# Kernel optimization log

Hardware: AMD Instinct MI355X
Metric: run time of the kernel (lower is better)

Reference implementation:

```python
import jax, jax.numpy as jnp
import numpy as np

B, S, D = 4, 2048, 1024


def setup_inputs() -> dict:
    key = jax.random.key(0)
    k1, k2 = jax.random.split(key)
    x = jax.random.normal(k1, (B, S, D), dtype=jnp.float32)
    W_qkv = jax.random.normal(k2, (D, 3 * D), dtype=jnp.float32) * 0.02
    # causal mask: 1 where attendable, 0 where masked (broadcast over batch)
    attention_mask = jnp.tril(jnp.ones((S, S), dtype=jnp.int32))[None, :, :]
    return {"input": x, "W_qkv": W_qkv, "attention_mask": attention_mask}


def reference(input, W_qkv, attention_mask):
    # fused QKV projection (nn.Linear, bias=False)
    qkv = jnp.einsum('bsd,de->bse', input, W_qkv)  # [B, S, 3D]
    q, k, v = jnp.split(qkv, 3, axis=-1)           # each [B, S, D]
    scale = 1.0 / jnp.sqrt(jnp.asarray(D, dtype=input.dtype))
    scores = jnp.einsum('bqd,bkd->bqk', q, k) * scale  # [B, S, S]
    neg_inf = jnp.finfo(scores.dtype).min
    scores = jnp.where(attention_mask == 0, neg_inf, scores)
    attn = jax.nn.softmax(scores, axis=-1)
    # dropout prob = 0.0 -> identity
    out = jnp.einsum('bqk,bkd->bqd', attn, v)      # [B, S, D]
    return out
```

## Files before the change

kernel.cpp:

```cpp
#include <hip/hip_runtime.h>
#include <hip/hip_bf16.h>


typedef __attribute__((ext_vector_type(8))) short short8;
typedef __attribute__((ext_vector_type(4))) short s16x4;
typedef __attribute__((ext_vector_type(4))) float f32x4;

__device__ __forceinline__ short f2bf(float f) {
  __hip_bfloat16 h = __float2bfloat16(f);
  return *reinterpret_cast<short*>(&h);
}

__device__ __forceinline__ void gll16(const void* g, void* l) {
  __builtin_amdgcn_global_load_lds((const __attribute__((address_space(1))) void*)g,
                                   (__attribute__((address_space(3))) void*)l,
                                   16, 0, 0);
}

__device__ __forceinline__ void gemm_core(const short* __restrict__ A,
                                          const short* __restrict__ Bt,
                                          int lda, int ldb,
                                          int row0, int col0, int kIters,
                                          f32x4 acc[4][4],
                                          short* lA, short* lB) {
  const int tid  = threadIdx.x;
  const int wave = tid >> 6;
  const int lane = tid & 63;
  const int quad = lane >> 4;
  const int l16  = lane & 15;

  const f32x4 zero = {0.f, 0.f, 0.f, 0.f};
#pragma unroll
  for (int i = 0; i < 4; ++i)
#pragma unroll
    for (int j = 0; j < 4; ++j) acc[i][j] = zero;

  const int srow = tid >> 3;
  const int gcol = ((tid & 7) ^ (srow & 7)) * 8;
  const short* A1 = A + (size_t)(row0 + srow) * lda + gcol;
  const short* A2 = A + (size_t)(row0 + srow + 32) * lda + gcol;
  const short* A3 = A + (size_t)(row0 + srow + 64) * lda + gcol;
  const short* A4 = A + (size_t)(row0 + srow + 96) * lda + gcol;
  const short* B1 = Bt + (size_t)(col0 + srow) * ldb + gcol;
  const short* B2 = Bt + (size_t)(col0 + srow + 32) * ldb + gcol;
  const short* B3 = Bt + (size_t)(col0 + srow + 64) * ldb + gcol;
  const short* B4 = Bt + (size_t)(col0 + srow + 96) * ldb + gcol;

  short* lA1 = lA + wave * 512;
  short* lA2 = lA + 2048 + wave * 512;
  short* lA3 = lA + 4096 + wave * 512;
  short* lA4 = lA + 6144 + wave * 512;
  short* lB1 = lB + wave * 512;
  short* lB2 = lB + 2048 + wave * 512;
  short* lB3 = lB + 4096 + wave * 512;
  short* lB4 = lB + 6144 + wave * 512;

  const int rswz  = l16 & 7;
  const int slot0 = (quad ^ rswz) * 8;
  const int slot1 = ((4 + quad) ^ rswz) * 8;
  const short* aRow = lA + ((wave >> 1) * 64 + l16) * 64;
  const short* bRow = lB + ((wave & 1) * 64 + l16) * 64;

  for (int it = 0; it < kIters; ++it) {
    const int k0 = it * 64;
    gll16(A1 + k0, lA1);
    gll16(A2 + k0, lA2);
    gll16(A3 + k0, lA3);
    gll16(A4 + k0, lA4);
    gll16(B1 + k0, lB1);
    gll16(B2 + k0, lB2);
    gll16(B3 + k0, lB3);
    gll16(B4 + k0, lB4);
    __syncthreads();

#pragma unroll
    for (int s = 0; s < 2; ++s) {
      const int so = s ? slot1 : slot0;
      short8 af[4], bfr[4];
#pragma unroll
      for (int i = 0; i < 4; ++i) af[i] = *(const short8*)(aRow + i * 1024 + so);
#pragma unroll
      for (int j = 0; j < 4; ++j) bfr[j] = *(const short8*)(bRow + j * 1024 + so);
#pragma unroll
      for (int i = 0; i < 4; ++i)
#pragma unroll
        for (int j = 0; j < 4; ++j)
          acc[i][j] = __builtin_amdgcn_mfma_f32_16x16x32_bf16(af[i], bfr[j], acc[i][j], 0, 0, 0);
    }
    __syncthreads();
  }
}

#define EPILOGUE_VARS                         \
  const int lane = threadIdx.x & 63;          \
  const int wave = threadIdx.x >> 6;          \
  const int quad = lane >> 4;                 \
  const int l16  = lane & 15;                 \
  const int rb   = (wave >> 1) * 64;          \
  const int cb   = (wave & 1) * 64;

__global__ __launch_bounds__(256) void setup_kernel(const float* __restrict__ X,
                                                    const float* __restrict__ W,
                                                    short* __restrict__ Xb,
                                                    short* __restrict__ Wt,
                                                    float* __restrict__ rs) {
  const int bid = blockIdx.x;
  if (bid < 8192) {
    const int i = (bid * 256 + threadIdx.x) * 4;
    const f32x4 v = *(const f32x4*)(X + i);
    s16x4 o;
    o.x = f2bf(v.x); o.y = f2bf(v.y); o.z = f2bf(v.z); o.w = f2bf(v.w);
    *(s16x4*)(Xb + i) = o;
  } else if (bid < 11264) {
    __shared__ float tile[32][33];
    const int r  = bid - 8192;
    const int ni = r % 96;
    const int ki = r / 96;
    const int tx = threadIdx.x & 31;
    const int ty = threadIdx.x >> 5;
#pragma unroll
    for (int rr = 0; rr < 4; ++rr)
      tile[ty + rr * 8][tx] = W[(size_t)(ki * 32 + ty + rr * 8) * 3072 + ni * 32 + tx];
    __syncthreads();
#pragma unroll
    for (int rr = 0; rr < 4; ++rr)
      Wt[(size_t)(ni * 32 + ty + rr * 8) * 1024 + ki * 32 + tx] = f2bf(tile[tx][ty + rr * 8]);
  } else {
    const int i = (bid - 11264) * 1024 + threadIdx.x * 4;
    const f32x4 zero = {0.f, 0.f, 0.f, 0.f};
    *(f32x4*)(rs + i) = zero;
  }
}

__global__ __launch_bounds__(256) void qkv_gemm_kernel(const short* __restrict__ Xb,
                                                       const short* __restrict__ Wt,
                                                       short* __restrict__ Q,
                                                       short* __restrict__ K,
                                                       short* __restrict__ Vt) {
  __shared__ short lA[8192], lB[8192];
  const int br = blockIdx.x / 24;
  const int bc = blockIdx.x % 24;
  f32x4 acc[4][4];
  gemm_core(Xb, Wt, 1024, 1024, br * 128, bc * 128, 16, acc, lA, lB);

  EPILOGUE_VARS
  const int rbase = br * 128 + rb;
  const int cbase = bc * 128 + cb;
  if (bc < 16) {
#pragma unroll
    for (int i = 0; i < 4; ++i)
#pragma unroll
      for (int j = 0; j < 4; ++j) {
        const int col = cbase + j * 16 + l16;
        short* dst = (col < 1024) ? Q : K;
        const int n = col & 1023;
#pragma unroll
        for (int r = 0; r < 4; ++r) {
          const int row = rbase + i * 16 + quad * 4 + r;
          dst[(size_t)row * 1024 + n] = f2bf(acc[i][j][r]);
        }
      }
  } else {
    const int b  = rbase >> 11;
    const int s0 = rbase & 2047;
    short* VtB = Vt + (size_t)b * 1024 * 2048;
#pragma unroll
    for (int i = 0; i < 4; ++i) {
      const int sb = s0 + i * 16 + quad * 4;
#pragma unroll
      for (int j = 0; j < 4; ++j) {
        const int d = cbase - 2048 + j * 16 + l16;
        s16x4 pk;
        pk.x = f2bf(acc[i][j][0]);
        pk.y = f2bf(acc[i][j][1]);
        pk.z = f2bf(acc[i][j][2]);
        pk.w = f2bf(acc[i][j][3]);
        *(s16x4*)(VtB + (size_t)d * 2048 + sb) = pk;
      }
    }
  }
}

__global__ __launch_bounds__(256) void qk_kernel(const short* __restrict__ Q,
                                                 const short* __restrict__ K,
                                                 short* __restrict__ E,
                                                 float* __restrict__ rs) {
  __shared__ short lA[8192], lB[8192];
  const int b  = blockIdx.x / 136;
  const int tt = blockIdx.x % 136;
  int qi = 0;
  while ((qi + 1) * (qi + 2) / 2 <= tt) qi++;
  const int ki = tt - qi * (qi + 1) / 2;

  f32x4 acc[4][4];
  const short* Qb = Q + (size_t)b * 2048 * 1024;
  const short* Kb = K + (size_t)b * 2048 * 1024;
  gemm_core(Qb, Kb, 1024, 1024, qi * 128, ki * 128, 16, acc, lA, lB);

  EPILOGUE_VARS
  short* Eb  = E + (size_t)b * 2048 * 2048;
  float* rsb = rs + b * 2048;
  const int rbase = qi * 128 + rb;
  const int cbase = ki * 128 + cb;
  const bool diag = (qi == ki);
#pragma unroll
  for (int i = 0; i < 4; ++i)
#pragma unroll
    for (int r = 0; r < 4; ++r) {
      const int row = rbase + i * 16 + quad * 4 + r;
      float partial = 0.f;
#pragma unroll
      for (int j = 0; j < 4; ++j) {
        const int col = cbase + j * 16 + l16;
        float e = __expf(acc[i][j][r] * 0.03125f);
        if (diag && col > row) e = 0.f;
        partial += e;
        Eb[(size_t)row * 2048 + col] = f2bf(e);
      }
      partial += __shfl_xor(partial, 1);
      partial += __shfl_xor(partial, 2);
      partial += __shfl_xor(partial, 4);
      partial += __shfl_xor(partial, 8);
      if (l16 == 0) atomicAdd(rsb + row, partial);
    }
}

__global__ __launch_bounds__(256) void pv_gemm_kernel(const short* __restrict__ E,
                                                      const short* __restrict__ Vt,
                                                      const float* __restrict__ rs,
                                                      float* __restrict__ out) {
  const int b  = blockIdx.x >> 7;
  const int r  = blockIdx.x & 127;
  const int qi = 15 - (r >> 3);
  const int dj = r & 7;

  __shared__ short lA[8192], lB[8192];
  f32x4 acc[4][4];
  const short* Eb  = E + (size_t)b * 2048 * 2048;
  const short* Vtb = Vt + (size_t)b * 1024 * 2048;
  gemm_core(Eb, Vtb, 2048, 2048, qi * 128, dj * 128, (qi + 1) * 2, acc, lA, lB);

  EPILOGUE_VARS
  float* ob = out + (size_t)b * 2048 * 1024;
  const float* rsb = rs + b * 2048;
  const int rbase = qi * 128 + rb;
  const int cbase = dj * 128 + cb;
#pragma unroll
  for (int i = 0; i < 4; ++i)
#pragma unroll
    for (int r2 = 0; r2 < 4; ++r2) {
      const int row = rbase + i * 16 + quad * 4 + r2;
      const float inv = 1.f / rsb[row];
#pragma unroll
      for (int j = 0; j < 4; ++j) {
        const int col = cbase + j * 16 + l16;
        ob[(size_t)row * 1024 + col] = acc[i][j][r2] * inv;
      }
    }
}

extern "C" void kernel_launch(void* const* d_in, const int* in_sizes, int n_in,
                              void* d_out, int out_size, void* d_ws, size_t ws_size,
                              hipStream_t stream) {
  const float* X = (const float*)d_in[0];
  const float* W = (const float*)d_in[1];
  float* out = (float*)d_out;
  char* w = (char*)d_ws;

  short* Xb = (short*)(w + 0);
  short* Wt = (short*)(w + 16777216);
  short* E  = (short*)(w + 0);
  float* rs = (float*)(w + 50331648);
  short* Q  = (short*)(w + 67108864);
  short* K  = (short*)(w + 83886080);
  short* Vt = (short*)(w + 100663296);

  hipLaunchKernelGGL(setup_kernel,    dim3(11272), dim3(256), 0, stream, X, W, Xb, Wt, rs);
  hipLaunchKernelGGL(qkv_gemm_kernel, dim3(1536),  dim3(256), 0, stream, Xb, Wt, Q, K, Vt);
  hipLaunchKernelGGL(qk_kernel,       dim3(544),   dim3(256), 0, stream, Q, K, E, rs);
  hipLaunchKernelGGL(pv_gemm_kernel,  dim3(512),   dim3(256), 0, stream, E, Vt, rs, out);
}
```

Measured before the change: 255.4 us.

## Fuse QK and PV kernels with per-row-block counters for cross-stage overlap

Merges the score/exp kernel and the PV GEMM into a single launch. The first 544 blocks compute QK tiles in descending query-block order and bump a per-(batch, query-block) counter with release semantics. The remaining blocks spin on that counter before running the PV GEMM for that row block. This removes a kernel boundary and lets PV work for the long rows start while QK for short rows is still running, at the cost of spin-waiting blocks that occupy CUs and rely on scheduling order to avoid deadlock. It also changes block ordering and interleaves batches.

Measured after the change: 407.7 us. +59.6%, slower.

```diff
diff --git a/kernel.cpp b/kernel.cpp
--- a/kernel.cpp
+++ b/kernel.cpp
@@ -103,7 +103,8 @@
                                                     const float* __restrict__ W,
                                                     short* __restrict__ Xb,
                                                     short* __restrict__ Wt,
-                                                    float* __restrict__ rs) {
+                                                    float* __restrict__ rs,
+                                                    int* __restrict__ cnt) {
   const int bid = blockIdx.x;
   if (bid < 8192) {
     const int i = (bid * 256 + threadIdx.x) * 4;
@@ -125,10 +126,12 @@
 #pragma unroll
     for (int rr = 0; rr < 4; ++rr)
       Wt[(size_t)(ni * 32 + ty + rr * 8) * 1024 + ki * 32 + tx] = f2bf(tile[tx][ty + rr * 8]);
-  } else {
+  } else if (bid < 11272) {
     const int i = (bid - 11264) * 1024 + threadIdx.x * 4;
     const f32x4 zero = {0.f, 0.f, 0.f, 0.f};
     *(f32x4*)(rs + i) = zero;
+  } else {
+    if (threadIdx.x < 64) cnt[threadIdx.x] = 0;
   }
 }
 
@@ -181,82 +184,99 @@
   }
 }
 
-__global__ __launch_bounds__(256) void qk_kernel(const short* __restrict__ Q,
-                                                 const short* __restrict__ K,
-                                                 short* __restrict__ E,
-                                                 float* __restrict__ rs) {
+__global__ __launch_bounds__(256, 3) void attn_kernel(const short* __restrict__ Q,
+                                                      const short* __restrict__ K,
+                                                      const short* __restrict__ Vt,
+                                                      short* __restrict__ E,
+                                                      float* __restrict__ rs,
+                                                      int* __restrict__ cnt,
+                                                      float* __restrict__ out) {
   __shared__ short lA[8192], lB[8192];
-  const int b  = blockIdx.x / 136;
-  const int tt = blockIdx.x % 136;
-  int qi = 0;
-  while ((qi + 1) * (qi + 2) / 2 <= tt) qi++;
-  const int ki = tt - qi * (qi + 1) / 2;
-
-  f32x4 acc[4][4];
-  const short* Qb = Q + (size_t)b * 2048 * 1024;
-  const short* Kb = K + (size_t)b * 2048 * 1024;
-  gemm_core(Qb, Kb, 1024, 1024, qi * 128, ki * 128, 16, acc, lA, lB);
-
-  EPILOGUE_VARS
-  short* Eb  = E + (size_t)b * 2048 * 2048;
-  float* rsb = rs + b * 2048;
-  const int rbase = qi * 128 + rb;
-  const int cbase = ki * 128 + cb;
-  const bool diag = (qi == ki);
-#pragma unroll
-  for (int i = 0; i < 4; ++i)
-#pragma unroll
-    for (int r = 0; r < 4; ++r) {
-      const int row = rbase + i * 16 + quad * 4 + r;
-      float partial = 0.f;
-#pragma unroll
-      for (int j = 0; j < 4; ++j) {
-        const int col = cbase + j * 16 + l16;
-        float e = __expf(acc[i][j][r] * 0.03125f);
-        if (diag && col > row) e = 0.f;
-        partial += e;
-        Eb[(size_t)row * 2048 + col] = f2bf(e);
-      }
-      partial += __shfl_xor(partial, 1);
-      partial += __shfl_xor(partial, 2);
-      partial += __shfl_xor(partial, 4);
-      partial += __shfl_xor(partial, 8);
-      if (l16 == 0) atomicAdd(rsb + row, partial);
+  if (blockIdx.x < 544) {
+    const int t = blockIdx.x >> 2;
+    const int b = blockIdx.x & 3;
+    int qi = 15, off = t;
+    while (off >= qi + 1) { off -= qi + 1; qi--; }
+    const int ki = off;
+
+    f32x4 acc[4][4];
+    const short* Qb = Q + (size_t)b * 2048 * 1024;
+    const short* Kb = K + (size_t)b * 2048 * 1024;
+    gemm_core(Qb, Kb, 1024, 1024, qi * 128, ki * 128, 16, acc, lA, lB);
+
+    EPILOGUE_VARS
+    short* Eb  = E + (size_t)b * 2048 * 2048;
+    float* rsb = rs + b * 2048;
+    const int rbase = qi * 128 + rb;
+    const int cbase = ki * 128 + cb;
+    const bool diag = (qi == ki);
+#pragma unroll
+    for (int i = 0; i < 4; ++i)
+#pragma unroll
+      for (int r = 0; r < 4; ++r) {
+        const int row = rbase + i * 16 + quad * 4 + r;
+        float partial = 0.f;
+#pragma unroll
+        for (int j = 0; j < 4; ++j) {
+          const int col = cbase + j * 16 + l16;
+          float e = __expf(acc[i][j][r] * 0.03125f);
+          if (diag && col > row) e = 0.f;
+          partial += e;
+          Eb[(size_t)row * 2048 + col] = f2bf(e);
+        }
+        partial += __shfl_xor(partial, 1);
+        partial += __shfl_xor(partial, 2);
+        partial += __shfl_xor(partial, 4);
+        partial += __shfl_xor(partial, 8);
+        if (l16 == 0) atomicAdd(rsb + row, partial);
+      }
+    __threadfence();
+    __syncthreads();
+    if (threadIdx.x == 0)
+      __hip_atomic_fetch_add(cnt + b * 16 + qi, 1,
+                             __ATOMIC_RELEASE, __HIP_MEMORY_SCOPE_AGENT);
+  } else {
+    const int r  = blockIdx.x - 544;
+    const int t  = r >> 2;
+    const int b  = r & 3;
+    const int qi = 15 - (t >> 3);
+    const int dj = t & 7;
+
+    if (threadIdx.x == 0) {
+      int guard = 0;
+      while (__hip_atomic_load(cnt + b * 16 + qi,
+                               __ATOMIC_ACQUIRE, __HIP_MEMORY_SCOPE_AGENT) < qi + 1) {
+        __builtin_amdgcn_s_sleep(8);
+        if (++guard > (1 << 22)) break;
+      }
     }
-}
-
-__global__ __launch_bounds__(256) void pv_gemm_kernel(const short* __restrict__ E,
-                                                      const short* __restrict__ Vt,
-                                                      const float* __restrict__ rs,
-                                                      float* __restrict__ out) {
-  const int b  = blockIdx.x >> 7;
-  const int r  = blockIdx.x & 127;
-  const int qi = 15 - (r >> 3);
-  const int dj = r & 7;
-
-  __shared__ short lA[8192], lB[8192];
-  f32x4 acc[4][4];
-  const short* Eb  = E + (size_t)b * 2048 * 2048;
-  const short* Vtb = Vt + (size_t)b * 1024 * 2048;
-  gemm_core(Eb, Vtb, 2048, 2048, qi * 128, dj * 128, (qi + 1) * 2, acc, lA, lB);
-
-  EPILOGUE_VARS
-  float* ob = out + (size_t)b * 2048 * 1024;
-  const float* rsb = rs + b * 2048;
-  const int rbase = qi * 128 + rb;
-  const int cbase = dj * 128 + cb;
-#pragma unroll
-  for (int i = 0; i < 4; ++i)
-#pragma unroll
-    for (int r2 = 0; r2 < 4; ++r2) {
-      const int row = rbase + i * 16 + quad * 4 + r2;
-      const float inv = 1.f / rsb[row];
-#pragma unroll
-      for (int j = 0; j < 4; ++j) {
-        const int col = cbase + j * 16 + l16;
-        ob[(size_t)row * 1024 + col] = acc[i][j][r2] * inv;
-      }
-    }
+    __syncthreads();
+    (void)__hip_atomic_load(cnt + b * 16 + qi,
+                            __ATOMIC_ACQUIRE, __HIP_MEMORY_SCOPE_AGENT);
+
+    f32x4 acc[4][4];
+    const short* Eb  = E + (size_t)b * 2048 * 2048;
+    const short* Vtb = Vt + (size_t)b * 1024 * 2048;
+    gemm_core(Eb, Vtb, 2048, 2048, qi * 128, dj * 128, (qi + 1) * 2, acc, lA, lB);
+
+    EPILOGUE_VARS
+    float* ob = out + (size_t)b * 2048 * 1024;
+    const float* rsb = rs + b * 2048;
+    const int rbase = qi * 128 + rb;
+    const int cbase = dj * 128 + cb;
+#pragma unroll
+    for (int i = 0; i < 4; ++i)
+#pragma unroll
+      for (int r2 = 0; r2 < 4; ++r2) {
+        const int row = rbase + i * 16 + quad * 4 + r2;
+        const float inv = 1.f / rsb[row];
+#pragma unroll
+        for (int j = 0; j < 4; ++j) {
+          const int col = cbase + j * 16 + l16;
+          ob[(size_t)row * 1024 + col] = acc[i][j][r2] * inv;
+        }
+      }
+  }
 }
 
 extern "C" void kernel_launch(void* const* d_in, const int* in_sizes, int n_in,
@@ -271,12 +291,12 @@
   short* Wt = (short*)(w + 16777216);
   short* E  = (short*)(w + 0);
   float* rs = (float*)(w + 50331648);
+  int*  cnt = (int*)(w + 50364416);
   short* Q  = (short*)(w + 67108864);
   short* K  = (short*)(w + 83886080);
   short* Vt = (short*)(w + 100663296);
 
-  hipLaunchKernelGGL(setup_kernel,    dim3(11272), dim3(256), 0, stream, X, W, Xb, Wt, rs);
+  hipLaunchKernelGGL(setup_kernel,    dim3(11273), dim3(256), 0, stream, X, W, Xb, Wt, rs, cnt);
   hipLaunchKernelGGL(qkv_gemm_kernel, dim3(1536),  dim3(256), 0, stream, Xb, Wt, Q, K, Vt);
-  hipLaunchKernelGGL(qk_kernel,       dim3(544),   dim3(256), 0, stream, Q, K, E, rs);
-  hipLaunchKernelGGL(pv_gemm_kernel,  dim3(512),   dim3(256), 0, stream, E, Vt, rs, out);
-}
+  hipLaunchKernelGGL(attn_kernel,     dim3(1056),  dim3(256), 0, stream, Q, K, Vt, E, rs, cnt, out);
+}
```

## Use 64x128 tiles with 128-thread blocks for QK and PV kernels

Applied to the files above, without the earlier changes.

Adds a 64-row by 128-column GEMM core with K-step 32 and two waves per block. The causal QK and PV kernels move to this smaller tile, launching twice as many blocks with batch interleaved into the block index and finer causal tiling along query rows. This is meant to raise occupancy and load balance on the triangular workload and to trim wasted work on diagonal tiles. In exchange, each block reuses less data per load and synchronises more often per unit of MFMA work.

Measured after the change: 253.5 us. Within noise of the previous version (-0.8%).

```diff
diff --git a/kernel.cpp b/kernel.cpp
--- a/kernel.cpp
+++ b/kernel.cpp
@@ -87,6 +87,68 @@
         for (int j = 0; j < 4; ++j)
           acc[i][j] = __builtin_amdgcn_mfma_f32_16x16x32_bf16(af[i], bfr[j], acc[i][j], 0, 0, 0);
     }
+    __syncthreads();
+  }
+}
+
+__device__ __forceinline__ void gemm_core64(const short* __restrict__ A,
+                                            const short* __restrict__ Bt,
+                                            int lda, int ldb,
+                                            int row0, int col0, int kIters,
+                                            f32x4 acc[4][4],
+                                            short* lA, short* lB) {
+  const int tid  = threadIdx.x;
+  const int wave = tid >> 6;
+  const int lane = tid & 63;
+  const int quad = lane >> 4;
+  const int l16  = lane & 15;
+
+  const f32x4 zero = {0.f, 0.f, 0.f, 0.f};
+#pragma unroll
+  for (int i = 0; i < 4; ++i)
+#pragma unroll
+    for (int j = 0; j < 4; ++j) acc[i][j] = zero;
+
+  const int srow = tid >> 2;
+  const int gcol = ((tid & 3) ^ ((srow >> 1) & 3)) * 8;
+  const short* A1 = A + (size_t)(row0 + srow) * lda + gcol;
+  const short* A2 = A + (size_t)(row0 + srow + 32) * lda + gcol;
+  const short* B1 = Bt + (size_t)(col0 + srow) * ldb + gcol;
+  const short* B2 = Bt + (size_t)(col0 + srow + 32) * ldb + gcol;
+  const short* B3 = Bt + (size_t)(col0 + srow + 64) * ldb + gcol;
+  const short* B4 = Bt + (size_t)(col0 + srow + 96) * ldb + gcol;
+
+  short* lA1 = lA + wave * 512;
+  short* lA2 = lA + 1024 + wave * 512;
+  short* lB1 = lB + wave * 512;
+  short* lB2 = lB + 1024 + wave * 512;
+  short* lB3 = lB + 2048 + wave * 512;
+  short* lB4 = lB + 3072 + wave * 512;
+
+  const int slot = ((quad ^ ((l16 >> 1) & 3))) * 8;
+  const short* aBase = lA + l16 * 32 + slot;
+  const short* bBase = lB + wave * 2048 + l16 * 32 + slot;
+
+  for (int it = 0; it < kIters; ++it) {
+    const int k0 = it * 32;
+    gll16(A1 + k0, lA1);
+    gll16(A2 + k0, lA2);
+    gll16(B1 + k0, lB1);
+    gll16(B2 + k0, lB2);
+    gll16(B3 + k0, lB3);
+    gll16(B4 + k0, lB4);
+    __syncthreads();
+
+    short8 af[4], bfr[4];
+#pragma unroll
+    for (int i = 0; i < 4; ++i) af[i] = *(const short8*)(aBase + i * 512);
+#pragma unroll
+    for (int j = 0; j < 4; ++j) bfr[j] = *(const short8*)(bBase + j * 512);
+#pragma unroll
+    for (int i = 0; i < 4; ++i)
+#pragma unroll
+      for (int j = 0; j < 4; ++j)
+        acc[i][j] = __builtin_amdgcn_mfma_f32_16x16x32_bf16(af[i], bfr[j], acc[i][j], 0, 0, 0);
     __syncthreads();
   }
 }
@@ -181,28 +243,31 @@
   }
 }
 
-__global__ __launch_bounds__(256) void qk_kernel(const short* __restrict__ Q,
+__global__ __launch_bounds__(128) void qk_kernel(const short* __restrict__ Q,
                                                  const short* __restrict__ K,
                                                  short* __restrict__ E,
                                                  float* __restrict__ rs) {
-  __shared__ short lA[8192], lB[8192];
-  const int b  = blockIdx.x / 136;
-  const int tt = blockIdx.x % 136;
-  int qi = 0;
-  while ((qi + 1) * (qi + 2) / 2 <= tt) qi++;
-  const int ki = tt - qi * (qi + 1) / 2;
+  __shared__ short lA[2048], lB[4096];
+  const int t = blockIdx.x >> 2;
+  const int b = blockIdx.x & 3;
+  int qi = 31, off = t;
+  while (off >= (qi >> 1) + 1) { off -= (qi >> 1) + 1; qi--; }
+  const int ki = off;
 
   f32x4 acc[4][4];
   const short* Qb = Q + (size_t)b * 2048 * 1024;
   const short* Kb = K + (size_t)b * 2048 * 1024;
-  gemm_core(Qb, Kb, 1024, 1024, qi * 128, ki * 128, 16, acc, lA, lB);
-
-  EPILOGUE_VARS
+  gemm_core64(Qb, Kb, 1024, 1024, qi * 64, ki * 128, 32, acc, lA, lB);
+
+  const int lane = threadIdx.x & 63;
+  const int wave = threadIdx.x >> 6;
+  const int quad = lane >> 4;
+  const int l16  = lane & 15;
   short* Eb  = E + (size_t)b * 2048 * 2048;
   float* rsb = rs + b * 2048;
-  const int rbase = qi * 128 + rb;
-  const int cbase = ki * 128 + cb;
-  const bool diag = (qi == ki);
+  const int rbase = qi * 64;
+  const int cbase = ki * 128 + wave * 64;
+  const bool diag = (ki == (qi >> 1));
 #pragma unroll
   for (int i = 0; i < 4; ++i)
 #pragma unroll
@@ -225,26 +290,29 @@
     }
 }
 
-__global__ __launch_bounds__(256) void pv_gemm_kernel(const short* __restrict__ E,
-                                                      const short* __restrict__ Vt,
-                                                      const float* __restrict__ rs,
-                                                      float* __restrict__ out) {
-  const int b  = blockIdx.x >> 7;
-  const int r  = blockIdx.x & 127;
-  const int qi = 15 - (r >> 3);
-  const int dj = r & 7;
-
-  __shared__ short lA[8192], lB[8192];
+__global__ __launch_bounds__(128) void pv_kernel(const short* __restrict__ E,
+                                                 const short* __restrict__ Vt,
+                                                 const float* __restrict__ rs,
+                                                 float* __restrict__ out) {
+  __shared__ short lA[2048], lB[4096];
+  const int t  = blockIdx.x >> 2;
+  const int b  = blockIdx.x & 3;
+  const int qi = 31 - (t >> 3);
+  const int dj = t & 7;
+
   f32x4 acc[4][4];
   const short* Eb  = E + (size_t)b * 2048 * 2048;
   const short* Vtb = Vt + (size_t)b * 1024 * 2048;
-  gemm_core(Eb, Vtb, 2048, 2048, qi * 128, dj * 128, (qi + 1) * 2, acc, lA, lB);
-
-  EPILOGUE_VARS
+  gemm_core64(Eb, Vtb, 2048, 2048, qi * 64, dj * 128, ((qi >> 1) + 1) * 4, acc, lA, lB);
+
+  const int lane = threadIdx.x & 63;
+  const int wave = threadIdx.x >> 6;
+  const int quad = lane >> 4;
+  const int l16  = lane & 15;
   float* ob = out + (size_t)b * 2048 * 1024;
   const float* rsb = rs + b * 2048;
-  const int rbase = qi * 128 + rb;
-  const int cbase = dj * 128 + cb;
+  const int rbase = qi * 64;
+  const int cbase = dj * 128 + wave * 64;
 #pragma unroll
   for (int i = 0; i < 4; ++i)
 #pragma unroll
@@ -277,6 +345,6 @@
 
   hipLaunchKernelGGL(setup_kernel,    dim3(11272), dim3(256), 0, stream, X, W, Xb, Wt, rs);
   hipLaunchKernelGGL(qkv_gemm_kernel, dim3(1536),  dim3(256), 0, stream, Xb, Wt, Q, K, Vt);
-  hipLaunchKernelGGL(qk_kernel,       dim3(544),   dim3(256), 0, stream, Q, K, E, rs);
-  hipLaunchKernelGGL(pv_gemm_kernel,  dim3(512),   dim3(256), 0, stream, E, Vt, rs, out);
-}
+  hipLaunchKernelGGL(qk_kernel,       dim3(1088),  dim3(128), 0, stream, Q, K, E, rs);
+  hipLaunchKernelGGL(pv_kernel,       dim3(1024),  dim3(128), 0, stream, E, Vt, rs, out);
+}
```
